# Kernel tuning notes

Measured on AMD Instinct MI355X. Metric: run time of the kernel, lower is better.

The kernel has to match this reference:

```python
import jax, jax.numpy as jnp
import numpy as np

N_BATCH, T = 65536, 256
SURROGATE_SLOPE = 5.0


def setup_inputs() -> dict:
    key = jax.random.key(0)
    k1, k2, k3, k4 = jax.random.split(key, 4)
    x = jax.random.normal(k1, (N_BATCH, T), dtype=jnp.float32)
    beta = jax.random.normal(k2, (), dtype=jnp.float32)
    threshold = jax.random.uniform(k3, (), dtype=jnp.float32)  # kept positive like a sane threshold init
    init_rand = jax.random.uniform(k4, (N_BATCH,), dtype=jnp.float32)  # torch.rand(N_batch)
    return {"x": x, "beta": beta, "threshold": threshold, "init_rand": init_rand}


def reference(x, beta, threshold, init_rand):
    # feasible_beta = sigmoid(beta); forward uses RAW threshold (not softplus)
    fb = jax.nn.sigmoid(beta)
    # memory init: rand * threshold.detach()
    m0 = init_rand * jax.lax.stop_gradient(threshold)

    def step(m, xt):
        m_new = fb * m + xt                      # StateUpdate
        surplus = m_new - threshold
        hard = (surplus >= 0).astype(x.dtype)    # forward spike
        soft = jax.nn.sigmoid(surplus * SURROGATE_SLOPE)  # surrogate grad path
        spike = jax.lax.stop_gradient(hard) + soft - jax.lax.stop_gradient(soft)
        m_post = m_new - jax.lax.stop_gradient(spike) * threshold  # StatePostupdate
        # torch records the PRE-step memory (initial m0, then previous post-update m)
        return m_post, (spike, m)

    _, (spikes_tn, mems_tn) = jax.lax.scan(step, m0, x.T)  # scan over T
    return spikes_tn.T, mems_tn.T  # each (N_batch, T)
```

## Files before the change

### kernel.cpp

```cpp
#include <hip/hip_runtime.h>
#include <math.h>


#define N_BATCH 65536
#define T_STEPS 256
#define ROWS    64
#define CHUNK   32
#define NCHUNK  (T_STEPS / CHUNK)
#define STRIDE  (CHUNK + 1)
#define XPL     8

#define LDS_FENCE() asm volatile("s_waitcnt lgkmcnt(0)" ::: "memory")

typedef float f32x4 __attribute__((ext_vector_type(4)));

__global__ __launch_bounds__(64) void snn_fwd_kernel(
    const float* __restrict__ x,
    const float* __restrict__ beta_p,
    const float* __restrict__ thr_p,
    const float* __restrict__ init_rand,
    float* __restrict__ out)
{
#pragma clang fp contract(off)
    __shared__ float xs[ROWS * STRIDE];
    __shared__ float ss[ROWS * STRIDE];
    __shared__ float ms[ROWS * STRIDE];

    const int t   = threadIdx.x;
    const int row = blockIdx.x * ROWS + t;

    const float thr = thr_p[0];
    const float fb = (float)(1.0 / (1.0 + exp(-(double)beta_p[0])));

    float m = init_rand[row] * thr;

    float* __restrict__ s_out = out;
    float* __restrict__ m_out = out + (size_t)N_BATCH * T_STEPS;

    const int k  = t & 7;
    const int r0 = t >> 3;

    {
        f32x4 xld[XPL];
#pragma unroll
        for (int q = 0; q < XPL; ++q) {
            const int rr = r0 + 8 * q;
            xld[q] = *reinterpret_cast<const f32x4*>(
                x + (size_t)(blockIdx.x * ROWS + rr) * T_STEPS + 4 * k);
        }
#pragma unroll
        for (int q = 0; q < XPL; ++q) {
            const int rr = r0 + 8 * q;
            const int la = rr * STRIDE + 4 * k;
            xs[la]     = xld[q].x; xs[la + 1] = xld[q].y;
            xs[la + 2] = xld[q].z; xs[la + 3] = xld[q].w;
        }
        LDS_FENCE();
    }

#pragma unroll
    for (int cc = 0; cc < NCHUNK; ++cc) {
        f32x4 xnext[XPL];
        if (cc + 1 < NCHUNK) {
#pragma unroll
            for (int q = 0; q < XPL; ++q) {
                const int rr = r0 + 8 * q;
                xnext[q] = *reinterpret_cast<const f32x4*>(
                    x + (size_t)(blockIdx.x * ROWS + rr) * T_STEPS
                      + (cc + 1) * CHUNK + 4 * k);
            }
        }

        float* __restrict__ xrow = xs + t * STRIDE;
        float* __restrict__ srow = ss + t * STRIDE;
        float* __restrict__ mrow = ms + t * STRIDE;
#pragma unroll
        for (int i = 0; i < CHUNK; ++i) {
            const float xv = xrow[i];
            mrow[i] = m;
            float prod = fb * m;
            float mn   = prod + xv;
            float su   = mn - thr;
            srow[i] = (su >= 0.0f) ? 1.0f : 0.0f;
            m = (su >= 0.0f) ? su : mn;
        }
        LDS_FENCE();

#pragma unroll
        for (int p = 0; p < 8; ++p) {
            const int rr = r0 + 8 * p;
            const int la = rr * STRIDE + 4 * k;
            f32x4 sv, mv;
            sv.x = ss[la];     sv.y = ss[la + 1];
            sv.z = ss[la + 2]; sv.w = ss[la + 3];
            mv.x = ms[la];     mv.y = ms[la + 1];
            mv.z = ms[la + 2]; mv.w = ms[la + 3];
            const size_t g = (size_t)(blockIdx.x * ROWS + rr) * T_STEPS
                           + cc * CHUNK + 4 * k;
            __builtin_nontemporal_store(sv, reinterpret_cast<f32x4*>(s_out + g));
            __builtin_nontemporal_store(mv, reinterpret_cast<f32x4*>(m_out + g));
        }
        LDS_FENCE();

        if (cc + 1 < NCHUNK) {
#pragma unroll
            for (int q = 0; q < XPL; ++q) {
                const int rr = r0 + 8 * q;
                const int la = rr * STRIDE + 4 * k;
                xs[la]     = xnext[q].x; xs[la + 1] = xnext[q].y;
                xs[la + 2] = xnext[q].z; xs[la + 3] = xnext[q].w;
            }
            LDS_FENCE();
        }
    }
}

extern "C" void kernel_launch(void* const* d_in, const int* in_sizes, int n_in,
                              void* d_out, int out_size, void* d_ws, size_t ws_size,
                              hipStream_t stream) {
    const float* x         = (const float*)d_in[0];
    const float* beta      = (const float*)d_in[1];
    const float* threshold = (const float*)d_in[2];
    const float* init_rand = (const float*)d_in[3];
    float* out             = (float*)d_out;

    const int threads = ROWS;
    const int blocks  = N_BATCH / ROWS;
    snn_fwd_kernel<<<blocks, threads, 0, stream>>>(x, beta, threshold, init_rand, out);
}
```

Before: 34.89 us.

## Replace padded LDS staging with XOR-swizzled 128-bit LDS accesses

Changes the shared-memory transpose buffers from a padded stride of 33 to an unpadded 32-wide layout with an XOR swizzle on 16-byte groups. All LDS reads and writes become f32x4 vector accesses instead of scalar ones, which cuts the LDS instruction count while the swizzle is meant to avoid bank conflicts. The explicit lgkmcnt fences are removed. With a single wavefront per block, correctness relies on the compiler inserting the needed waits itself.

```diff
diff --git a/kernel.cpp b/kernel.cpp
--- a/kernel.cpp
+++ b/kernel.cpp
@@ -7,12 +7,13 @@
 #define ROWS    64
 #define CHUNK   32
 #define NCHUNK  (T_STEPS / CHUNK)
-#define STRIDE  (CHUNK + 1)
-#define XPL     8
-
-#define LDS_FENCE() asm volatile("s_waitcnt lgkmcnt(0)" ::: "memory")
+#define GPR     (CHUNK / 4)
 
 typedef float f32x4 __attribute__((ext_vector_type(4)));
+
+__device__ __forceinline__ int swz(int r, int g) {
+    return r * CHUNK + 4 * (g ^ (r & 7));
+}
 
 __global__ __launch_bounds__(64) void snn_fwd_kernel(
     const float* __restrict__ x,
@@ -22,9 +23,9 @@
     float* __restrict__ out)
 {
 #pragma clang fp contract(off)
-    __shared__ float xs[ROWS * STRIDE];
-    __shared__ float ss[ROWS * STRIDE];
-    __shared__ float ms[ROWS * STRIDE];
+    __shared__ float xs[ROWS * CHUNK];
+    __shared__ float ss[ROWS * CHUNK];
+    __shared__ float ms[ROWS * CHUNK];
 
     const int t   = threadIdx.x;
     const int row = blockIdx.x * ROWS + t;
@@ -41,29 +42,24 @@
     const int r0 = t >> 3;
 
     {
-        f32x4 xld[XPL];
+        f32x4 xld[GPR];
 #pragma unroll
-        for (int q = 0; q < XPL; ++q) {
+        for (int q = 0; q < GPR; ++q) {
             const int rr = r0 + 8 * q;
             xld[q] = *reinterpret_cast<const f32x4*>(
                 x + (size_t)(blockIdx.x * ROWS + rr) * T_STEPS + 4 * k);
         }
 #pragma unroll
-        for (int q = 0; q < XPL; ++q) {
-            const int rr = r0 + 8 * q;
-            const int la = rr * STRIDE + 4 * k;
-            xs[la]     = xld[q].x; xs[la + 1] = xld[q].y;
-            xs[la + 2] = xld[q].z; xs[la + 3] = xld[q].w;
-        }
-        LDS_FENCE();
+        for (int q = 0; q < GPR; ++q)
+            *reinterpret_cast<f32x4*>(xs + swz(r0 + 8 * q, k)) = xld[q];
     }
 
 #pragma unroll
     for (int cc = 0; cc < NCHUNK; ++cc) {
-        f32x4 xnext[XPL];
+        f32x4 xnext[GPR];
         if (cc + 1 < NCHUNK) {
 #pragma unroll
-            for (int q = 0; q < XPL; ++q) {
+            for (int q = 0; q < GPR; ++q) {
                 const int rr = r0 + 8 * q;
                 xnext[q] = *reinterpret_cast<const f32x4*>(
                     x + (size_t)(blockIdx.x * ROWS + rr) * T_STEPS
@@ -71,46 +67,42 @@
             }
         }
 
-        float* __restrict__ xrow = xs + t * STRIDE;
-        float* __restrict__ srow = ss + t * STRIDE;
-        float* __restrict__ mrow = ms + t * STRIDE;
+        f32x4 xv[GPR];
 #pragma unroll
-        for (int i = 0; i < CHUNK; ++i) {
-            const float xv = xrow[i];
-            mrow[i] = m;
-            float prod = fb * m;
-            float mn   = prod + xv;
-            float su   = mn - thr;
-            srow[i] = (su >= 0.0f) ? 1.0f : 0.0f;
-            m = (su >= 0.0f) ? su : mn;
-        }
-        LDS_FENCE();
+        for (int i = 0; i < GPR; ++i)
+            xv[i] = *reinterpret_cast<const f32x4*>(xs + swz(t, i));
 
 #pragma unroll
-        for (int p = 0; p < 8; ++p) {
+        for (int i = 0; i < GPR; ++i) {
+            f32x4 sv4, mv4;
+#pragma unroll
+            for (int j = 0; j < 4; ++j) {
+                mv4[j] = m;
+                float prod = fb * m;
+                float mn   = prod + xv[i][j];
+                float su   = mn - thr;
+                sv4[j] = (su >= 0.0f) ? 1.0f : 0.0f;
+                m = (su >= 0.0f) ? su : mn;
+            }
+            *reinterpret_cast<f32x4*>(ss + swz(t, i)) = sv4;
+            *reinterpret_cast<f32x4*>(ms + swz(t, i)) = mv4;
+        }
+
+#pragma unroll
+        for (int p = 0; p < GPR; ++p) {
             const int rr = r0 + 8 * p;
-            const int la = rr * STRIDE + 4 * k;
-            f32x4 sv, mv;
-            sv.x = ss[la];     sv.y = ss[la + 1];
-            sv.z = ss[la + 2]; sv.w = ss[la + 3];
-            mv.x = ms[la];     mv.y = ms[la + 1];
-            mv.z = ms[la + 2]; mv.w = ms[la + 3];
+            const f32x4 sv = *reinterpret_cast<const f32x4*>(ss + swz(rr, k));
+            const f32x4 mv = *reinterpret_cast<const f32x4*>(ms + swz(rr, k));
             const size_t g = (size_t)(blockIdx.x * ROWS + rr) * T_STEPS
                            + cc * CHUNK + 4 * k;
             __builtin_nontemporal_store(sv, reinterpret_cast<f32x4*>(s_out + g));
             __builtin_nontemporal_store(mv, reinterpret_cast<f32x4*>(m_out + g));
         }
-        LDS_FENCE();
 
         if (cc + 1 < NCHUNK) {
 #pragma unroll
-            for (int q = 0; q < XPL; ++q) {
-                const int rr = r0 + 8 * q;
-                const int la = rr * STRIDE + 4 * k;
-                xs[la]     = xnext[q].x; xs[la + 1] = xnext[q].y;
-                xs[la + 2] = xnext[q].z; xs[la + 3] = xnext[q].w;
-            }
-            LDS_FENCE();
+            for (int q = 0; q < GPR; ++q)
+                *reinterpret_cast<f32x4*>(xs + swz(r0 + 8 * q, k)) = xnext[q];
         }
     }
 }
```

Measured after the change: 34.96 us. No clear change (+0.2%).
